# Performance work log

Measured on AMD Instinct MI355X. Metric: run time of the kernel, lower is better.

## Reference

```python
import jax, jax.numpy as jnp
import numpy as np

N = 32768       # total nodes across the batch of graphs
E = 524288      # total edges
D = 512         # feature dim (dimensions = [512, 512, 512])
G = 512         # number of graphs (64 nodes each)


def setup_inputs() -> dict:
    key = jax.random.key(0)
    ks = jax.random.split(key, 16)
    inp = {
        'feat': jax.random.normal(ks[0], (N, D), jnp.float32),
        'src': jax.random.randint(ks[1], (E,), 0, N, jnp.int32),
        'dst': jax.random.randint(ks[2], (E,), 0, N, jnp.int32),
        'adj_vals': jax.random.uniform(ks[3], (E,), jnp.float32),
        'graph_ids': (jnp.arange(N, dtype=jnp.int32) // (N // G)),
        'W0': jax.random.normal(ks[4], (D, D), jnp.float32) * 0.05,
        'b0': jnp.zeros((D,), jnp.float32),
        'W1': jax.random.normal(ks[5], (D, D), jnp.float32) * 0.05,
        'b1': jnp.zeros((D,), jnp.float32),
        'gW1': jax.random.normal(ks[6], (D, D), jnp.float32) * 0.05,
        'gb1': jnp.zeros((D,), jnp.float32),
        'gW2': jax.random.normal(ks[7], (D, D), jnp.float32) * 0.05,
        'gb2': jnp.zeros((D,), jnp.float32),
        'gW3': jax.random.normal(ks[8], (D, D), jnp.float32) * 0.05,
        'gb3': jnp.zeros((D,), jnp.float32),
        'gWs': jax.random.normal(ks[9], (D, D), jnp.float32) * 0.05,
        'gbs': jnp.zeros((D,), jnp.float32),
    }
    return inp


def reference(feat, src, dst, adj_vals, graph_ids,
              W0, b0, W1, b1,
              gW1, gb1, gW2, gb2, gW3, gb3, gWs, gbs):
    # GCN layer: act(A_hat @ (X W) + b), A_hat given as weighted edge list
    def gcn(h, W, b, act):
        support = h @ W                              # [N, D]
        msg = adj_vals[:, None] * support[src]       # [E, D]
        agg = jax.ops.segment_sum(msg, dst, num_segments=N)
        return act(agg + b)

    h = gcn(feat, W0, b0, jax.nn.relu)               # hidden layer, act=relu
    h = gcn(h, W1, b1, lambda x: x)                  # last layer, identity act

    # pooling: per-graph mean readout -> sigmoid -> repeat-expand back to nodes
    ones = jnp.ones((N, 1), h.dtype)
    counts = jax.ops.segment_sum(ones, graph_ids, num_segments=G)   # [G, 1]
    pooled = jax.ops.segment_sum(h, graph_ids, num_segments=G) / counts
    g = jax.nn.sigmoid(pooled)[graph_ids]            # [N, D] repeat-expanded

    z = jax.nn.relu(g @ gW1 + gb1)
    z = jax.nn.relu(z @ gW2 + gb2)
    z = jax.nn.relu(z @ gW3 + gb3)
    return z + (g @ gWs + gbs)
```

## Files before the change

### kernel.cpp

```cpp
#include <hip/hip_runtime.h>

typedef unsigned int u32;
typedef unsigned short u16;

typedef __attribute__((ext_vector_type(8))) __bf16 bf16x8;
typedef __attribute__((ext_vector_type(4))) float f32x4;
typedef __attribute__((ext_vector_type(2))) float f32x2;
typedef __attribute__((ext_vector_type(4))) u32 u32x4;

#define N_NODES 32768
#define N_EDGES 524288
#define DIM 512
#define N_GRAPHS 512
#define ECAP 1536

__device__ __forceinline__ u16 f2b(float f) {
  union { float f; u32 u; } v; v.f = f;
  u32 r = v.u + 0x7FFFu + ((v.u >> 16) & 1u);
  return (u16)(r >> 16);
}
__device__ __forceinline__ u32 pack2(float a, float b) {
  return (u32)f2b(a) | ((u32)f2b(b) << 16);
}
__device__ __forceinline__ float blo(u32 u) { union { u32 u; float f; } v; v.u = u << 16; return v.f; }
__device__ __forceinline__ float bhi(u32 u) { union { u32 u; float f; } v; v.u = u & 0xFFFF0000u; return v.f; }
__device__ __forceinline__ float b2f(u16 u) { union { u32 u; float f; } v; v.u = ((u32)u) << 16; return v.f; }

__device__ __forceinline__ void async16(const void* g, void* l) {
  __builtin_amdgcn_global_load_lds(
      (const __attribute__((address_space(1))) u32*)g,
      (__attribute__((address_space(3))) u32*)l, 16, 0, 0);
}

__device__ __forceinline__ void acc8(f32x2* a, u32x4 raw, float v) {
  f32x2 v2 = {v, v};
  a[0] += v2 * f32x2{blo(raw.x), bhi(raw.x)};
  a[1] += v2 * f32x2{blo(raw.y), bhi(raw.y)};
  a[2] += v2 * f32x2{blo(raw.z), bhi(raw.z)};
  a[3] += v2 * f32x2{blo(raw.w), bhi(raw.w)};
}

__global__ void k_f32_to_bf16(const float* __restrict__ in, u16* __restrict__ out, int n8) {
  int i = blockIdx.x * 256 + threadIdx.x;
  if (i >= n8) return;
  const float4* p = (const float4*)in;
  float4 a = p[2 * i], b = p[2 * i + 1];
  uint4 o;
  o.x = pack2(a.x, a.y); o.y = pack2(a.z, a.w);
  o.z = pack2(b.x, b.y); o.w = pack2(b.z, b.w);
  ((uint4*)out)[i] = o;
}

struct WPack {
  const float* src[6];
  u16* dst[6];
};
__global__ void k_transpose6(WPack p) {
  __shared__ float tile[32][33];
  const float* W = p.src[blockIdx.z];
  u16* Wt = p.dst[blockIdx.z];
  int bx = blockIdx.x * 32, by = blockIdx.y * 32;
  int tx = threadIdx.x, ty = threadIdx.y;
  #pragma unroll
  for (int i = 0; i < 4; i++)
    tile[ty + 8 * i][tx] = W[(size_t)(by + ty + 8 * i) * DIM + bx + tx];
  __syncthreads();
  #pragma unroll
  for (int i = 0; i < 4; i++)
    Wt[(size_t)(bx + ty + 8 * i) * DIM + by + tx] = f2b(tile[tx][ty + 8 * i]);
}

__global__ void k_hist(const int* __restrict__ dst, int* __restrict__ counts) {
  int i = blockIdx.x * 256 + threadIdx.x;
  if (i < N_EDGES) atomicAdd(&counts[dst[i]], 1);
}

__global__ void k_scan(const int* __restrict__ counts, int* __restrict__ offsets,
                       int* __restrict__ cursor) {
  __shared__ int part[1024];
  int t = threadIdx.x;
  int base = t * 32;
  int loc[32];
  int s = 0;
  #pragma unroll
  for (int i = 0; i < 32; i++) { loc[i] = s; s += counts[base + i]; }
  part[t] = s;
  __syncthreads();
  for (int off = 1; off < 1024; off <<= 1) {
    int v = (t >= off) ? part[t - off] : 0;
    __syncthreads();
    part[t] += v;
    __syncthreads();
  }
  int excl = (t == 0) ? 0 : part[t - 1];
  #pragma unroll
  for (int i = 0; i < 32; i++) { int o = excl + loc[i]; offsets[base + i] = o; cursor[base + i] = o; }
  if (t == 1023) offsets[N_NODES] = excl + s;
}

__global__ void k_fill(const int* __restrict__ src, const int* __restrict__ dst,
                       const float* __restrict__ vals, int* __restrict__ cursor,
                       int2* __restrict__ epack) {
  int i = blockIdx.x * 256 + threadIdx.x;
  if (i >= N_EDGES) return;
  int d = dst[i];
  int p = atomicAdd(&cursor[d], 1);
  epack[p] = make_int2(src[i], __float_as_int(vals[i]));
}

template <bool RELU, bool BIAS, bool ADDEND, bool OUTF32>
__global__ __launch_bounds__(256)
void k_gemm_bt(const u16* __restrict__ A, const u16* __restrict__ Bt,
               const float* __restrict__ bias, const u16* __restrict__ addend,
               void* __restrict__ Cout, int M, int Nout, int K) {
  __shared__ __align__(16) u16 As[128 * 32];
  __shared__ __align__(16) u16 Bs[128 * 32];
  const int tid = threadIdx.x;
  const int l = tid & 63;
  const int w = tid >> 6;
  const int mBase = blockIdx.x * 128;
  const int nBase = blockIdx.y * 128;
  const int wm = (w >> 1) * 64;
  const int wn = (w & 1) * 64;
  const int lrow = l >> 2;
  const int lcol = (l & 3) * 8;
  const int q = l >> 4;
  const int r = l & 15;
  f32x4 acc[4][4] = {};

  for (int k0 = 0; k0 < K; k0 += 32) {
    #pragma unroll
    for (int p = 0; p < 2; p++) {
      int row = w * 32 + p * 16 + lrow;
      async16(A + (size_t)(mBase + row) * K + k0 + lcol, (char*)As + w * 2048 + p * 1024);
      async16(Bt + (size_t)(nBase + row) * K + k0 + lcol, (char*)Bs + w * 2048 + p * 1024);
    }
    __syncthreads();
    bf16x8 af[4], bfr[4];
    #pragma unroll
    for (int i = 0; i < 4; i++) af[i] = *(const bf16x8*)&As[(wm + i * 16 + r) * 32 + q * 8];
    #pragma unroll
    for (int j = 0; j < 4; j++) bfr[j] = *(const bf16x8*)&Bs[(wn + j * 16 + r) * 32 + q * 8];
    #pragma unroll
    for (int i = 0; i < 4; i++)
      #pragma unroll
      for (int j = 0; j < 4; j++)
        acc[i][j] = __builtin_amdgcn_mfma_f32_16x16x32_bf16(af[i], bfr[j], acc[i][j], 0, 0, 0);
    __syncthreads();
  }

  #pragma unroll
  for (int i = 0; i < 4; i++) {
    #pragma unroll
    for (int j = 0; j < 4; j++) {
      int col = nBase + wn + j * 16 + r;
      float bv = BIAS ? bias[col] : 0.0f;
      #pragma unroll
      for (int reg = 0; reg < 4; reg++) {
        int rowg = mBase + wm + i * 16 + q * 4 + reg;
        float v = acc[i][j][reg] + bv;
        if (ADDEND) v += b2f(addend[(size_t)rowg * Nout + col]);
        if (RELU) v = fmaxf(v, 0.0f);
        if (OUTF32) ((float*)Cout)[(size_t)rowg * Nout + col] = v;
        else ((u16*)Cout)[(size_t)rowg * Nout + col] = f2b(v);
      }
    }
  }
}

template <bool RELU, bool POOL>
__global__ __launch_bounds__(256)
void k_agg(const u16* __restrict__ support, const int* __restrict__ offsets,
           const int2* __restrict__ epack, const float* __restrict__ bias,
           u16* __restrict__ outp) {
  __shared__ int2 eLds[ECAP];
  __shared__ float poolLds[4][64];
  const int chunk = blockIdx.x & 7;
  const int cidx  = blockIdx.x >> 3;
  const int rowBase = cidx * 64;
  const int e0b = offsets[rowBase];
  const int nb = offsets[rowBase + 64] - e0b;
  for (int i = threadIdx.x; i < min(nb, ECAP); i += 256)
    eLds[i] = epack[e0b + i];
  __syncthreads();

  const int wi = threadIdx.x >> 6;
  const int l  = threadIdx.x & 63;
  const int grp = l >> 3;
  const int li  = l & 7;
  const int colOff = chunk * 64 + li * 8;
  const u16* spc = support + colOff;

  f32x2 b[4];
  {
    const float4* bp = (const float4*)(bias + colOff);
    float4 x = bp[0], y = bp[1];
    b[0] = f32x2{x.x, x.y}; b[1] = f32x2{x.z, x.w};
    b[2] = f32x2{y.x, y.y}; b[3] = f32x2{y.z, y.w};
  }

  f32x2 psum[4] = {};

  #pragma unroll
  for (int pass = 0; pass < 2; pass++) {
    int r = rowBase + wi * 16 + pass * 8 + grp;
    int re0 = offsets[r] - e0b;
    int deg = offsets[r + 1] - e0b - re0;

    f32x2 a[4] = {b[0], b[1], b[2], b[3]};

    if (nb <= ECAP) {
      int i = 0;
      for (; i + 4 <= deg; i += 4) {
        int2 p0 = eLds[re0 + i];
        int2 p1 = eLds[re0 + i + 1];
        int2 p2 = eLds[re0 + i + 2];
        int2 p3 = eLds[re0 + i + 3];
        u32x4 r0 = *(const u32x4*)(spc + (size_t)p0.x * DIM);
        u32x4 r1 = *(const u32x4*)(spc + (size_t)p1.x * DIM);
        u32x4 r2 = *(const u32x4*)(spc + (size_t)p2.x * DIM);
        u32x4 r3 = *(const u32x4*)(spc + (size_t)p3.x * DIM);
        acc8(a, r0, __int_as_float(p0.y));
        acc8(a, r1, __int_as_float(p1.y));
        acc8(a, r2, __int_as_float(p2.y));
        acc8(a, r3, __int_as_float(p3.y));
      }
      for (; i < deg; i++) {
        int2 p = eLds[re0 + i];
        u32x4 raw = *(const u32x4*)(spc + (size_t)p.x * DIM);
        acc8(a, raw, __int_as_float(p.y));
      }
    } else {
      for (int i = 0; i < deg; i++) {
        int gi = re0 + i;
        int2 p = (gi < ECAP) ? eLds[gi] : epack[e0b + gi];
        u32x4 raw = *(const u32x4*)(spc + (size_t)p.x * DIM);
        acc8(a, raw, __int_as_float(p.y));
      }
    }

    if (POOL) {
      #pragma unroll
      for (int i = 0; i < 4; i++) psum[i] += a[i];
    } else {
      if (RELU) {
        #pragma unroll
        for (int i = 0; i < 4; i++) {
          a[i].x = fmaxf(a[i].x, 0.0f);
          a[i].y = fmaxf(a[i].y, 0.0f);
        }
      }
      u32x4 o;
      o.x = pack2(a[0].x, a[0].y); o.y = pack2(a[1].x, a[1].y);
      o.z = pack2(a[2].x, a[2].y); o.w = pack2(a[3].x, a[3].y);
      *(u32x4*)(outp + (size_t)r * DIM + colOff) = o;
    }
  }

  if (POOL) {
    #pragma unroll
    for (int k = 0; k < 4; k++) {
      psum[k].x += __shfl_xor(psum[k].x, 8);  psum[k].y += __shfl_xor(psum[k].y, 8);
      psum[k].x += __shfl_xor(psum[k].x, 16); psum[k].y += __shfl_xor(psum[k].y, 16);
      psum[k].x += __shfl_xor(psum[k].x, 32); psum[k].y += __shfl_xor(psum[k].y, 32);
    }
    if (grp == 0) {
      #pragma unroll
      for (int k = 0; k < 4; k++) {
        poolLds[wi][li * 8 + 2 * k]     = psum[k].x;
        poolLds[wi][li * 8 + 2 * k + 1] = psum[k].y;
      }
    }
    __syncthreads();
    if (threadIdx.x < 64) {
      int cc = threadIdx.x;
      float s = poolLds[0][cc] + poolLds[1][cc] + poolLds[2][cc] + poolLds[3][cc];
      float m = s * (1.0f / 64.0f);
      float sg = 1.0f / (1.0f + expf(-m));
      outp[(size_t)cidx * DIM + chunk * 64 + cc] = f2b(sg);
    }
  }
}

__global__ void k_expand(const float* __restrict__ small, float* __restrict__ out) {
  int i = blockIdx.x * 256 + threadIdx.x;
  int col4 = i & 127;
  int node = i >> 7;
  float4 v = ((const float4*)small)[((node >> 6) << 7) + col4];
  ((float4*)out)[i] = v;
}

extern "C" void kernel_launch(void* const* d_in, const int* in_sizes, int n_in,
                              void* d_out, int out_size, void* d_ws, size_t ws_size,
                              hipStream_t stream) {
  const float* feat = (const float*)d_in[0];
  const int* src    = (const int*)d_in[1];
  const int* dst    = (const int*)d_in[2];
  const float* adj  = (const float*)d_in[3];
  const float* W0  = (const float*)d_in[5];
  const float* b0  = (const float*)d_in[6];
  const float* W1  = (const float*)d_in[7];
  const float* b1  = (const float*)d_in[8];
  const float* gW1 = (const float*)d_in[9];
  const float* gb1 = (const float*)d_in[10];
  const float* gW2 = (const float*)d_in[11];
  const float* gb2 = (const float*)d_in[12];
  const float* gW3 = (const float*)d_in[13];
  const float* gb3 = (const float*)d_in[14];
  const float* gWs = (const float*)d_in[15];
  const float* gbs = (const float*)d_in[16];

  char* ws = (char*)d_ws;
  size_t off = 0;
  auto alloc = [&](size_t bytes) -> void* {
    void* p = ws + off;
    off = (off + bytes + 255) & ~(size_t)255;
    return p;
  };
  u16* bufA = (u16*)alloc((size_t)N_NODES * DIM * 2);
  u16* bufB = (u16*)alloc((size_t)N_NODES * DIM * 2);
  u16* wt[6];
  for (int i = 0; i < 6; i++) wt[i] = (u16*)alloc((size_t)DIM * DIM * 2);
  int* counts   = (int*)alloc((size_t)N_NODES * 4);
  int* offsets  = (int*)alloc((size_t)(N_NODES + 1) * 4);
  int* cursor   = (int*)alloc((size_t)N_NODES * 4);
  int2* epack   = (int2*)alloc((size_t)N_EDGES * 8);
  u16* gfeat    = (u16*)alloc((size_t)N_GRAPHS * DIM * 2);
  u16* z1       = (u16*)alloc((size_t)N_GRAPHS * DIM * 2);
  u16* z2       = (u16*)alloc((size_t)N_GRAPHS * DIM * 2);
  u16* z3       = (u16*)alloc((size_t)N_GRAPHS * DIM * 2);
  float* osmall = (float*)alloc((size_t)N_GRAPHS * DIM * 4);

  (void)hipMemsetAsync(counts, 0, (size_t)N_NODES * 4, stream);

  k_f32_to_bf16<<<(N_NODES * DIM / 8) / 256, 256, 0, stream>>>(feat, bufA, N_NODES * DIM / 8);

  WPack wp;
  wp.src[0] = W0; wp.src[1] = W1; wp.src[2] = gW1; wp.src[3] = gW2; wp.src[4] = gW3; wp.src[5] = gWs;
  for (int i = 0; i < 6; i++) wp.dst[i] = wt[i];
  k_transpose6<<<dim3(16, 16, 6), dim3(32, 8), 0, stream>>>(wp);

  k_hist<<<N_EDGES / 256, 256, 0, stream>>>(dst, counts);
  k_scan<<<1, 1024, 0, stream>>>(counts, offsets, cursor);
  k_fill<<<N_EDGES / 256, 256, 0, stream>>>(src, dst, adj, cursor, epack);

  dim3 gBig(N_NODES / 128, DIM / 128);
  k_gemm_bt<false, false, false, false><<<gBig, 256, 0, stream>>>(bufA, wt[0], nullptr, nullptr, bufB, N_NODES, DIM, DIM);
  k_agg<true, false><<<4096, 256, 0, stream>>>(bufB, offsets, epack, b0, bufA);
  k_gemm_bt<false, false, false, false><<<gBig, 256, 0, stream>>>(bufA, wt[1], nullptr, nullptr, bufB, N_NODES, DIM, DIM);
  k_agg<false, true><<<4096, 256, 0, stream>>>(bufB, offsets, epack, b1, gfeat);

  dim3 gSmall(N_GRAPHS / 128, DIM / 128);
  k_gemm_bt<true, true, false, false><<<gSmall, 256, 0, stream>>>(gfeat, wt[2], gb1, nullptr, z1, N_GRAPHS, DIM, DIM);
  k_gemm_bt<true, true, false, false><<<gSmall, 256, 0, stream>>>(z1, wt[3], gb2, nullptr, z2, N_GRAPHS, DIM, DIM);
  k_gemm_bt<true, true, false, false><<<gSmall, 256, 0, stream>>>(z2, wt[4], gb3, nullptr, z3, N_GRAPHS, DIM, DIM);
  k_gemm_bt<false, true, true, true><<<gSmall, 256, 0, stream>>>(gfeat, wt[5], gbs, z3, osmall, N_GRAPHS, DIM, DIM);

  k_expand<<<(N_NODES * DIM / 4) / 256, 256, 0, stream>>>(osmall, (float*)d_out);
}
```

Before: 443.7 us.

## Reorder second GCN layer to pool before projecting, shrink small GEMMs, fuse prep kernels

Because the second GCN layer is linear and mean pooling commutes with the weight product, the code now aggregates the hidden features first, pools them per graph, and only then multiplies the 512x512 pooled matrix by W1, adding bias and sigmoid in that GEMM. This removes the full N x D second projection GEMM. The conversion, weight transpose and histogram kernels are merged into one launch, the scan uses vectorized loads and stores, and the small GEMMs use 64x64 tiles so more blocks run. Rounding differs slightly because the bf16 round trip now happens at a different point.

```diff
diff --git a/kernel.cpp b/kernel.cpp
--- a/kernel.cpp
+++ b/kernel.cpp
@@ -13,6 +13,8 @@
 #define DIM 512
 #define N_GRAPHS 512
 #define ECAP 1536
+#define NB_CONV 8192
+#define NB_TR 1536
 
 __device__ __forceinline__ u16 f2b(float f) {
   union { float f; u32 u; } v; v.f = f;
@@ -40,50 +42,60 @@
   a[3] += v2 * f32x2{blo(raw.w), bhi(raw.w)};
 }
 
-__global__ void k_f32_to_bf16(const float* __restrict__ in, u16* __restrict__ out, int n8) {
-  int i = blockIdx.x * 256 + threadIdx.x;
-  if (i >= n8) return;
-  const float4* p = (const float4*)in;
-  float4 a = p[2 * i], b = p[2 * i + 1];
-  uint4 o;
-  o.x = pack2(a.x, a.y); o.y = pack2(a.z, a.w);
-  o.z = pack2(b.x, b.y); o.w = pack2(b.z, b.w);
-  ((uint4*)out)[i] = o;
-}
-
 struct WPack {
   const float* src[6];
   u16* dst[6];
 };
-__global__ void k_transpose6(WPack p) {
+__global__ __launch_bounds__(256)
+void k_prep(const float* __restrict__ feat, u16* __restrict__ featb, WPack wp,
+            const int* __restrict__ dstv, int* __restrict__ counts) {
   __shared__ float tile[32][33];
-  const float* W = p.src[blockIdx.z];
-  u16* Wt = p.dst[blockIdx.z];
-  int bx = blockIdx.x * 32, by = blockIdx.y * 32;
-  int tx = threadIdx.x, ty = threadIdx.y;
-  #pragma unroll
-  for (int i = 0; i < 4; i++)
-    tile[ty + 8 * i][tx] = W[(size_t)(by + ty + 8 * i) * DIM + bx + tx];
-  __syncthreads();
-  #pragma unroll
-  for (int i = 0; i < 4; i++)
-    Wt[(size_t)(bx + ty + 8 * i) * DIM + by + tx] = f2b(tile[tx][ty + 8 * i]);
-}
-
-__global__ void k_hist(const int* __restrict__ dst, int* __restrict__ counts) {
-  int i = blockIdx.x * 256 + threadIdx.x;
-  if (i < N_EDGES) atomicAdd(&counts[dst[i]], 1);
+  const int bid = blockIdx.x, tid = threadIdx.x;
+  if (bid < NB_CONV) {
+    int i = bid * 256 + tid;
+    const float4* p = (const float4*)feat;
+    float4 a = p[2 * i], b = p[2 * i + 1];
+    uint4 o;
+    o.x = pack2(a.x, a.y); o.y = pack2(a.z, a.w);
+    o.z = pack2(b.x, b.y); o.w = pack2(b.z, b.w);
+    ((uint4*)featb)[i] = o;
+  } else if (bid < NB_CONV + NB_TR) {
+    int idx = bid - NB_CONV;
+    int bz = idx >> 8, rem = idx & 255, by = rem >> 4, bx = rem & 15;
+    const float* W = wp.src[bz];
+    u16* Wt = wp.dst[bz];
+    int tx = tid & 31, ty = tid >> 5;
+    int bx32 = bx * 32, by32 = by * 32;
+    #pragma unroll
+    for (int i = 0; i < 4; i++)
+      tile[ty + 8 * i][tx] = W[(size_t)(by32 + ty + 8 * i) * DIM + bx32 + tx];
+    __syncthreads();
+    #pragma unroll
+    for (int i = 0; i < 4; i++)
+      Wt[(size_t)(bx32 + ty + 8 * i) * DIM + by32 + tx] = f2b(tile[tx][ty + 8 * i]);
+  } else {
+    int i = (bid - NB_CONV - NB_TR) * 256 + tid;
+    atomicAdd(&counts[dstv[i]], 1);
+  }
 }
 
 __global__ void k_scan(const int* __restrict__ counts, int* __restrict__ offsets,
                        int* __restrict__ cursor) {
   __shared__ int part[1024];
   int t = threadIdx.x;
-  int base = t * 32;
+  const int4* c4 = (const int4*)counts;
+  int4 cv[8];
+  #pragma unroll
+  for (int j = 0; j < 8; j++) cv[j] = c4[t * 8 + j];
   int loc[32];
   int s = 0;
   #pragma unroll
-  for (int i = 0; i < 32; i++) { loc[i] = s; s += counts[base + i]; }
+  for (int j = 0; j < 8; j++) {
+    loc[4 * j + 0] = s; s += cv[j].x;
+    loc[4 * j + 1] = s; s += cv[j].y;
+    loc[4 * j + 2] = s; s += cv[j].z;
+    loc[4 * j + 3] = s; s += cv[j].w;
+  }
   part[t] = s;
   __syncthreads();
   for (int off = 1; off < 1024; off <<= 1) {
@@ -94,7 +106,12 @@
   }
   int excl = (t == 0) ? 0 : part[t - 1];
   #pragma unroll
-  for (int i = 0; i < 32; i++) { int o = excl + loc[i]; offsets[base + i] = o; cursor[base + i] = o; }
+  for (int j = 0; j < 8; j++) {
+    int4 o = make_int4(excl + loc[4 * j], excl + loc[4 * j + 1],
+                       excl + loc[4 * j + 2], excl + loc[4 * j + 3]);
+    ((int4*)offsets)[t * 8 + j] = o;
+    ((int4*)cursor)[t * 8 + j] = o;
+  }
   if (t == 1023) offsets[N_NODES] = excl + s;
 }
 
@@ -108,11 +125,9 @@
   epack[p] = make_int2(src[i], __float_as_int(vals[i]));
 }
 
-template <bool RELU, bool BIAS, bool ADDEND, bool OUTF32>
 __global__ __launch_bounds__(256)
 void k_gemm_bt(const u16* __restrict__ A, const u16* __restrict__ Bt,
-               const float* __restrict__ bias, const u16* __restrict__ addend,
-               void* __restrict__ Cout, int M, int Nout, int K) {
+               u16* __restrict__ Cout, int M, int Nout, int K) {
   __shared__ __align__(16) u16 As[128 * 32];
   __shared__ __align__(16) u16 Bs[128 * 32];
   const int tid = threadIdx.x;
@@ -154,13 +169,65 @@
     #pragma unroll
     for (int j = 0; j < 4; j++) {
       int col = nBase + wn + j * 16 + r;
-      float bv = BIAS ? bias[col] : 0.0f;
+      #pragma unroll
+      for (int reg = 0; reg < 4; reg++) {
+        int rowg = mBase + wm + i * 16 + q * 4 + reg;
+        Cout[(size_t)rowg * Nout + col] = f2b(acc[i][j][reg]);
+      }
+    }
+  }
+}
+
+template <bool RELU, bool ADDEND, bool OUTF32, bool SIGMOID>
+__global__ __launch_bounds__(256)
+void k_gemm_small(const u16* __restrict__ A, const u16* __restrict__ Bt,
+                  const float* __restrict__ bias, const u16* __restrict__ addend,
+                  void* __restrict__ Cout, int Nout, int K) {
+  __shared__ __align__(16) u16 As[64 * 32];
+  __shared__ __align__(16) u16 Bs[64 * 32];
+  const int tid = threadIdx.x;
+  const int l = tid & 63;
+  const int w = tid >> 6;
+  const int mBase = blockIdx.x * 64;
+  const int nBase = blockIdx.y * 64;
+  const int wm = (w >> 1) * 32;
+  const int wn = (w & 1) * 32;
+  const int lrow = tid >> 2;
+  const int lcol = (tid & 3) * 8;
+  const int q = l >> 4;
+  const int r = l & 15;
+  f32x4 acc[2][2] = {};
+
+  for (int k0 = 0; k0 < K; k0 += 32) {
+    async16(A + (size_t)(mBase + lrow) * K + k0 + lcol, (char*)As + tid * 16);
+    async16(Bt + (size_t)(nBase + lrow) * K + k0 + lcol, (char*)Bs + tid * 16);
+    __syncthreads();
+    bf16x8 af[2], bfr[2];
+    #pragma unroll
+    for (int i = 0; i < 2; i++) af[i] = *(const bf16x8*)&As[(wm + i * 16 + r) * 32 + q * 8];
+    #pragma unroll
+    for (int j = 0; j < 2; j++) bfr[j] = *(const bf16x8*)&Bs[(wn + j * 16 + r) * 32 + q * 8];
+    #pragma unroll
+    for (int i = 0; i < 2; i++)
+      #pragma unroll
+      for (int j = 0; j < 2; j++)
+        acc[i][j] = __builtin_amdgcn_mfma_f32_16x16x32_bf16(af[i], bfr[j], acc[i][j], 0, 0, 0);
+    __syncthreads();
+  }
+
+  #pragma unroll
+  for (int i = 0; i < 2; i++) {
+    #pragma unroll
+    for (int j = 0; j < 2; j++) {
+      int col = nBase + wn + j * 16 + r;
+      float bv = bias[col];
       #pragma unroll
       for (int reg = 0; reg < 4; reg++) {
         int rowg = mBase + wm + i * 16 + q * 4 + reg;
         float v = acc[i][j][reg] + bv;
         if (ADDEND) v += b2f(addend[(size_t)rowg * Nout + col]);
         if (RELU) v = fmaxf(v, 0.0f);
+        if (SIGMOID) v = 1.0f / (1.0f + expf(-v));
         if (OUTF32) ((float*)Cout)[(size_t)rowg * Nout + col] = v;
         else ((u16*)Cout)[(size_t)rowg * Nout + col] = f2b(v);
       }
@@ -191,8 +258,8 @@
   const int colOff = chunk * 64 + li * 8;
   const u16* spc = support + colOff;
 
-  f32x2 b[4];
-  {
+  f32x2 b[4] = {};
+  if (!POOL) {
     const float4* bp = (const float4*)(bias + colOff);
     float4 x = bp[0], y = bp[1];
     b[0] = f32x2{x.x, x.y}; b[1] = f32x2{x.z, x.w};
@@ -275,9 +342,7 @@
     if (threadIdx.x < 64) {
       int cc = threadIdx.x;
       float s = poolLds[0][cc] + poolLds[1][cc] + poolLds[2][cc] + poolLds[3][cc];
-      float m = s * (1.0f / 64.0f);
-      float sg = 1.0f / (1.0f + expf(-m));
-      outp[(size_t)cidx * DIM + chunk * 64 + cc] = f2b(sg);
+      outp[(size_t)cidx * DIM + chunk * 64 + cc] = f2b(s * (1.0f / 64.0f));
     }
   }
 }
@@ -325,6 +390,7 @@
   int* offsets  = (int*)alloc((size_t)(N_NODES + 1) * 4);
   int* cursor   = (int*)alloc((size_t)N_NODES * 4);
   int2* epack   = (int2*)alloc((size_t)N_EDGES * 8);
+  u16* qb       = (u16*)alloc((size_t)N_GRAPHS * DIM * 2);
   u16* gfeat    = (u16*)alloc((size_t)N_GRAPHS * DIM * 2);
   u16* z1       = (u16*)alloc((size_t)N_GRAPHS * DIM * 2);
   u16* z2       = (u16*)alloc((size_t)N_GRAPHS * DIM * 2);
@@ -333,28 +399,23 @@
 
   (void)hipMemsetAsync(counts, 0, (size_t)N_NODES * 4, stream);
 
-  k_f32_to_bf16<<<(N_NODES * DIM / 8) / 256, 256, 0, stream>>>(feat, bufA, N_NODES * DIM / 8);
-
   WPack wp;
   wp.src[0] = W0; wp.src[1] = W1; wp.src[2] = gW1; wp.src[3] = gW2; wp.src[4] = gW3; wp.src[5] = gWs;
   for (int i = 0; i < 6; i++) wp.dst[i] = wt[i];
-  k_transpose6<<<dim3(16, 16, 6), dim3(32, 8), 0, stream>>>(wp);
-
-  k_hist<<<N_EDGES / 256, 256, 0, stream>>>(dst, counts);
+
+  k_prep<<<NB_CONV + NB_TR + N_EDGES / 256, 256, 0, stream>>>(feat, bufA, wp, dst, counts);
   k_scan<<<1, 1024, 0, stream>>>(counts, offsets, cursor);
   k_fill<<<N_EDGES / 256, 256, 0, stream>>>(src, dst, adj, cursor, epack);
 
-  dim3 gBig(N_NODES / 128, DIM / 128);
-  k_gemm_bt<false, false, false, false><<<gBig, 256, 0, stream>>>(bufA, wt[0], nullptr, nullptr, bufB, N_NODES, DIM, DIM);
+  k_gemm_bt<<<dim3(N_NODES / 128, DIM / 128), 256, 0, stream>>>(bufA, wt[0], bufB, N_NODES, DIM, DIM);
   k_agg<true, false><<<4096, 256, 0, stream>>>(bufB, offsets, epack, b0, bufA);
-  k_gemm_bt<false, false, false, false><<<gBig, 256, 0, stream>>>(bufA, wt[1], nullptr, nullptr, bufB, N_NODES, DIM, DIM);
-  k_agg<false, true><<<4096, 256, 0, stream>>>(bufB, offsets, epack, b1, gfeat);
-
-  dim3 gSmall(N_GRAPHS / 128, DIM / 128);
-  k_gemm_bt<true, true, false, false><<<gSmall, 256, 0, stream>>>(gfeat, wt[2], gb1, nullptr, z1, N_GRAPHS, DIM, DIM);
-  k_gemm_bt<true, true, false, false><<<gSmall, 256, 0, stream>>>(z1, wt[3], gb2, nullptr, z2, N_GRAPHS, DIM, DIM);
-  k_gemm_bt<true, true, false, false><<<gSmall, 256, 0, stream>>>(z2, wt[4], gb3, nullptr, z3, N_GRAPHS, DIM, DIM);
-  k_gemm_bt<false, true, true, true><<<gSmall, 256, 0, stream>>>(gfeat, wt[5], gbs, z3, osmall, N_GRAPHS, DIM, DIM);
+  k_agg<false, true><<<4096, 256, 0, stream>>>(bufA, offsets, epack, nullptr, qb);
+  k_gemm_small<false, false, false, true><<<dim3(8, 8), 256, 0, stream>>>(qb, wt[1], b1, nullptr, gfeat, DIM, DIM);
+
+  k_gemm_small<true, false, false, false><<<dim3(8, 8), 256, 0, stream>>>(gfeat, wt[2], gb1, nullptr, z1, DIM, DIM);
+  k_gemm_small<true, false, false, false><<<dim3(8, 8), 256, 0, stream>>>(z1, wt[3], gb2, nullptr, z2, DIM, DIM);
+  k_gemm_small<true, false, false, false><<<dim3(8, 8), 256, 0, stream>>>(z2, wt[4], gb3, nullptr, z3, DIM, DIM);
+  k_gemm_small<false, true, true, false><<<dim3(8, 8), 256, 0, stream>>>(gfeat, wt[5], gbs, z3, osmall, DIM, DIM);
 
   k_expand<<<(N_NODES * DIM / 4) / 256, 256, 0, stream>>>(osmall, (float*)d_out);
 }
```

Result: faster. 390.6 us (-12.0%).
